# Performance work log

Measured on AMD Instinct MI355X. Metric: run time of the kernel, lower is better.

The kernel has to match this reference:

```python
import jax, jax.numpy as jnp
import numpy as np

M_LEN = 1024
BATCH = 16384


def setup_inputs() -> dict:
    key = jax.random.key(0)
    k0, k1, k2, k3, kw = jax.random.split(key, 5)
    mod0 = jax.random.normal(k0, (BATCH, M_LEN), dtype=jnp.float32)
    mod1 = jax.random.normal(k1, (BATCH, M_LEN), dtype=jnp.float32)
    mod2 = jax.random.normal(k2, (BATCH, M_LEN), dtype=jnp.float32)
    mod3 = jax.random.normal(k3, (BATCH, M_LEN), dtype=jnp.float32)
    # simulate missing modality for first quarter of patients (exercises rescale path)
    mod1 = mod1.at[: BATCH // 4].set(0.0)
    W = jax.random.normal(kw, (M_LEN, M_LEN), dtype=jnp.float32) * (1.0 / np.sqrt(M_LEN))
    return {"mod0": mod0, "mod1": mod1, "mod2": mod2, "mod3": mod3, "W": W}


def reference(mod0, mod1, mod2, mod3, W):
    ndata = jnp.stack([mod0, mod1, mod2, mod3])          # [M, B, L]
    scores = jnp.einsum("mbl,kl->mbk", ndata, W)          # Linear (no bias): x @ W.T
    attention_weights = jax.nn.softmax(scores, axis=0)    # softmax over modalities
    fused = jnp.sum(ndata * attention_weights, axis=0)    # [B, L]
    # vectorized replacement of per-patient python loop:
    # count modalities whose sum is exactly zero; if >0, scale row by (count+1)
    zero_dims = jnp.sum(jnp.sum(ndata, axis=2) == 0.0, axis=0)          # [B] int
    scaler = jnp.where(zero_dims > 0, zero_dims + 1, 1).astype(fused.dtype)
    return fused * scaler[:, None]
```

## Files before the change

kernel.cpp:

```cpp
#include <hip/hip_runtime.h>
#include <hip/hip_bf16.h>

#define M_LEN 1024
#define BATCH 16384

#define BM 128
#define BN 128
#define BK 64
#define THREADS 256

#define BM2 256
#define BN2 256
#define GTHREADS 512

typedef __attribute__((ext_vector_type(8))) short bf16x8;
typedef __attribute__((ext_vector_type(4))) float f32x4;
typedef unsigned short ushort_t;


__device__ __forceinline__ ushort_t bf16_rne(float f) {
    unsigned u = __float_as_uint(f);
    unsigned r = u + 0x7FFFu + ((u >> 16) & 1u);
    return (ushort_t)(r >> 16);
}

__device__ __forceinline__ float bf16_to_f(ushort_t u) {
    return __uint_as_float(((unsigned)u) << 16);
}

__device__ __forceinline__ unsigned pack2(float lo, float hi) {
    return __builtin_amdgcn_perm(__float_as_uint(hi), __float_as_uint(lo), 0x07060302u);
}

__device__ __forceinline__ void gload_lds16(const void* g, void* l) {
    __builtin_amdgcn_global_load_lds(
        (const __attribute__((address_space(1))) unsigned int*)g,
        (__attribute__((address_space(3))) unsigned int*)l,
        16, 0, 0);
}

__device__ __forceinline__ float4 ntload4(const float4* p) {
    f32x4 v = __builtin_nontemporal_load((const f32x4*)p);
    return make_float4(v.x, v.y, v.z, v.w);
}

__global__ __launch_bounds__(THREADS) void convert_pass(
    const float* __restrict__ mod0, const float* __restrict__ mod1,
    const float* __restrict__ mod2, const float* __restrict__ mod3,
    const float* __restrict__ W,
    ushort_t* __restrict__ Ab, ushort_t* __restrict__ Wb, int* __restrict__ zf)
{
    const int blk  = blockIdx.x;
    const int wave = threadIdx.x >> 6;
    const int lane = threadIdx.x & 63;

    if (blk < BATCH) {
        const int b = blk, m = wave;
        const float* mp = (m == 0) ? mod0 : (m == 1) ? mod1 : (m == 2) ? mod2 : mod3;
        const float4* row = (const float4*)(mp + (size_t)b * M_LEN);
        ushort_t* dst = Ab + ((size_t)b * 4 + m) * M_LEN;
        unsigned orr = 0u;
        #pragma unroll
        for (int j = 0; j < 4; ++j) {
            float4 v = ntload4(&row[j * 64 + lane]);
            orr |= (__float_as_uint(v.x) | __float_as_uint(v.y) |
                    __float_as_uint(v.z) | __float_as_uint(v.w)) << 1;
            ushort4 o;
            o.x = bf16_rne(v.x); o.y = bf16_rne(v.y);
            o.z = bf16_rne(v.z); o.w = bf16_rne(v.w);
            ((ushort4*)dst)[j * 64 + lane] = o;
        }
        const int nz = __any(orr != 0u);
        if (lane == 0) zf[b * 4 + m] = nz ? 0 : 1;
    } else {
        const int r = (blk - BATCH) * 4 + wave;
        const float4* row = (const float4*)(W + (size_t)r * M_LEN);
        ushort_t* dst = Wb + (size_t)r * M_LEN;
        #pragma unroll
        for (int j = 0; j < 4; ++j) {
            float4 v = row[j * 64 + lane];
            ushort4 o;
            o.x = bf16_rne(v.x); o.y = bf16_rne(v.y);
            o.z = bf16_rne(v.z); o.w = bf16_rne(v.w);
            ((ushort4*)dst)[j * 64 + lane] = o;
        }
    }
}

__global__ __launch_bounds__(GTHREADS, 2) void gemm_fused3(
    const ushort_t* __restrict__ Ab, const ushort_t* __restrict__ Wb,
    const int* __restrict__ zf, float* __restrict__ out)
{
    __shared__ __align__(16) ushort_t As0[BM2 * BK];
    __shared__ __align__(16) ushort_t Bs0[BN2 * BK];
    __shared__ __align__(16) ushort_t As1[BM2 * BK];
    __shared__ __align__(16) ushort_t Bs1[BN2 * BK];
    __shared__ float scalerS[BM2 / 4];

    const int t    = threadIdx.x;
    const int lane = t & 63;
    const int wave = t >> 6;
    const int quad = lane >> 4;
    const int ln15 = lane & 15;
    const int wm   = wave >> 2;
    const int wn   = wave & 3;

    const int bid  = blockIdx.x;
    const int wid  = (bid & 7) * 128 + (bid >> 3);
    const int colb = wid & 3;
    const int rowb = wid >> 2;
    const int row0 = rowb * BM2;
    const int col0 = colb * BN2;

    if (t < 64) {
        const int4 f = ((const int4*)zf)[rowb * 64 + t];
        const int z = f.x + f.y + f.z + f.w;
        scalerS[t] = (z > 0) ? (float)(z + 1) : 1.0f;
    }

    const int rloc = (lane >> 3);
    const int c8   = (lane & 7) ^ rloc;
    const ushort_t* aP[4];
    const ushort_t* bP[4];
    unsigned dstOff[4];
    #pragma unroll
    for (int q = 0; q < 4; ++q) {
        const int r = wave * 32 + q * 8 + rloc;
        aP[q] = Ab + (size_t)(row0 + r) * M_LEN + c8 * 8;
        bP[q] = Wb + (size_t)(col0 + r) * M_LEN + c8 * 8;
        dstOff[q] = (unsigned)((wave * 32 + q * 8) * 64);
    }

    #define STAGE(AD, BD)                                                   \
        do {                                                                \
            _Pragma("unroll")                                               \
            for (int q = 0; q < 4; ++q) {                                   \
                gload_lds16(aP[q], (AD) + dstOff[q]);                       \
                aP[q] += BK;                                                \
            }                                                               \
            _Pragma("unroll")                                               \
            for (int q = 0; q < 4; ++q) {                                   \
                gload_lds16(bP[q], (BD) + dstOff[q]);                       \
                bP[q] += BK;                                                \
            }                                                               \
        } while (0)

    f32x4 acc[8][4];
    #pragma unroll
    for (int i = 0; i < 8; ++i)
        #pragma unroll
        for (int j = 0; j < 4; ++j)
            acc[i][j] = (f32x4){0.f, 0.f, 0.f, 0.f};

    const unsigned slotB   = (unsigned)(quad ^ (ln15 & 7));
    const unsigned aRowOff = (unsigned)((wm * 128 + ln15) * 64);
    const unsigned bRowOff = (unsigned)((wn * 64 + ln15) * 64);

    auto compute = [&](const ushort_t* As_, const ushort_t* Bs_) {
        #pragma unroll
        for (int ks = 0; ks < 2; ++ks) {
            const unsigned slot8 = (slotB ^ (unsigned)(ks * 4)) * 8u;
            bf16x8 af[8], bfr[4];
            #pragma unroll
            for (int i = 0; i < 8; ++i)
                af[i] = *(const bf16x8*)(&As_[aRowOff + i * 1024 + slot8]);
            #pragma unroll
            for (int j = 0; j < 4; ++j)
                bfr[j] = *(const bf16x8*)(&Bs_[bRowOff + j * 1024 + slot8]);
            #pragma unroll
            for (int i = 0; i < 8; ++i)
                #pragma unroll
                for (int j = 0; j < 4; ++j)
                    acc[i][j] = __builtin_amdgcn_mfma_f32_16x16x32_bf16(
                        af[i], bfr[j], acc[i][j], 0, 0, 0);
        }
    };

    STAGE(As0, Bs0);
    STAGE(As1, Bs1);
    asm volatile("s_waitcnt vmcnt(8) lgkmcnt(0)" ::: "memory");
    __builtin_amdgcn_s_barrier();

    #pragma unroll 1
    for (int t2 = 0; t2 < 7; ++t2) {
        compute(As0, Bs0);
        __builtin_amdgcn_s_barrier();
        STAGE(As0, Bs0);
        asm volatile("s_waitcnt vmcnt(8)" ::: "memory");
        __builtin_amdgcn_s_barrier();

        compute(As1, Bs1);
        __builtin_amdgcn_s_barrier();
        STAGE(As1, Bs1);
        asm volatile("s_waitcnt vmcnt(8)" ::: "memory");
        __builtin_amdgcn_s_barrier();
    }
    compute(As0, Bs0);
    asm volatile("s_waitcnt vmcnt(0)" ::: "memory");
    __builtin_amdgcn_s_barrier();
    compute(As1, Bs1);

    #pragma unroll
    for (int i = 0; i < 8; ++i) {
        const int bl = wm * 32 + i * 4 + quad;
        const int b  = rowb * 64 + bl;
        const float scal = scalerS[bl];
        const ushort_t* xr = Ab + (size_t)b * 4 * M_LEN;
        #pragma unroll
        for (int j = 0; j < 4; ++j) {
            const int k = col0 + wn * 64 + j * 16 + ln15;
            const float x0 = bf16_to_f(xr[k]);
            const float x1 = bf16_to_f(xr[M_LEN + k]);
            const float x2 = bf16_to_f(xr[2 * M_LEN + k]);
            const float x3 = bf16_to_f(xr[3 * M_LEN + k]);
            const f32x4 s = acc[i][j];
            const float mx = fmaxf(fmaxf(s.x, s.y), fmaxf(s.z, s.w));
            const float e0 = __expf(s.x - mx);
            const float e1 = __expf(s.y - mx);
            const float e2 = __expf(s.z - mx);
            const float e3 = __expf(s.w - mx);
            const float num = e0 * x0 + e1 * x1 + e2 * x2 + e3 * x3;
            const float v = num * scal / (e0 + e1 + e2 + e3);
            __builtin_nontemporal_store(v, &out[(size_t)b * M_LEN + k]);
        }
    }
    #undef STAGE
}

__global__ __launch_bounds__(THREADS) void fused_modal_attn(
    const float* __restrict__ mod0, const float* __restrict__ mod1,
    const float* __restrict__ mod2, const float* __restrict__ mod3,
    const float* __restrict__ W, float* __restrict__ out)
{
    __shared__ __align__(16) unsigned short As[BM * BK];
    __shared__ __align__(16) unsigned short Bs[BN * BK];
    __shared__ unsigned rowOr[BM];
    __shared__ float scalerS[BM / 4];

    const int t    = threadIdx.x;
    const int lane = t & 63;
    const int wave = t >> 6;
    const int quad = lane >> 4;
    const int ln15 = lane & 15;
    const int wm   = wave >> 1;
    const int wn   = wave & 1;

    const int colb = blockIdx.x;
    const int rowb = blockIdx.y;
    const int row0 = rowb * BM;
    const int col0 = colb * BN;

    if (t < BM) rowOr[t] = 0u;

    const int sr  = t >> 3;
    const int scl = t & 7;

    const float* ap[4];
    const float* bp[4];
    unsigned ldsOff[4];
    unsigned orAcc[4] = {0u, 0u, 0u, 0u};
    #pragma unroll
    for (int j = 0; j < 4; ++j) {
        const int r  = j * 32 + sr;
        const int gr = row0 + r;
        const int b  = gr >> 2;
        const int m  = gr & 3;
        const float* mp = (m == 0) ? mod0 : (m == 1) ? mod1 : (m == 2) ? mod2 : mod3;
        ap[j] = mp + (size_t)b * M_LEN + scl * 8;
        bp[j] = W + (size_t)(col0 + r) * M_LEN + scl * 8;
        ldsOff[j] = (unsigned)(r * 64 + ((scl ^ (r & 7)) * 8));
    }

    f32x4 acc[4][4];
    #pragma unroll
    for (int i = 0; i < 4; ++i)
        #pragma unroll
        for (int j = 0; j < 4; ++j)
            acc[i][j] = (f32x4){0.f, 0.f, 0.f, 0.f};

    const unsigned slotB   = (unsigned)(quad ^ (ln15 & 7));
    const unsigned aRowOff = (unsigned)((wm * 64 + ln15) * 64);
    const unsigned bRowOff = (unsigned)((wn * 64 + ln15) * 64);

    for (int it = 0; it < 16; ++it) {
        __syncthreads();
        #pragma unroll
        for (int j = 0; j < 4; ++j) {
            const float4* pa = (const float4*)ap[j];
            const float4* pb = (const float4*)bp[j];
            float4 a0 = pa[0], a1 = pa[1];
            float4 b0 = pb[0], b1 = pb[1];
            ap[j] += BK; bp[j] += BK;

            unsigned pA0 = pack2(a0.x, a0.y), pA1 = pack2(a0.z, a0.w);
            unsigned pA2 = pack2(a1.x, a1.y), pA3 = pack2(a1.z, a1.w);
            orAcc[j] |= (pA0 | pA1) | (pA2 | pA3);
            *(uint4*)(&As[ldsOff[j]]) = make_uint4(pA0, pA1, pA2, pA3);

            unsigned pB0 = pack2(b0.x, b0.y), pB1 = pack2(b0.z, b0.w);
            unsigned pB2 = pack2(b1.x, b1.y), pB3 = pack2(b1.z, b1.w);
            *(uint4*)(&Bs[ldsOff[j]]) = make_uint4(pB0, pB1, pB2, pB3);
        }
        __syncthreads();
        #pragma unroll
        for (int ks = 0; ks < 2; ++ks) {
            const unsigned slot8 = (slotB ^ (unsigned)(ks * 4)) * 8u;
            bf16x8 af[4], bfr[4];
            #pragma unroll
            for (int i = 0; i < 4; ++i)
                af[i] = *(const bf16x8*)(&As[aRowOff + i * 1024 + slot8]);
            #pragma unroll
            for (int j = 0; j < 4; ++j)
                bfr[j] = *(const bf16x8*)(&Bs[bRowOff + j * 1024 + slot8]);
            #pragma unroll
            for (int i = 0; i < 4; ++i)
                #pragma unroll
                for (int j = 0; j < 4; ++j)
                    acc[i][j] = __builtin_amdgcn_mfma_f32_16x16x32_bf16(
                        af[i], bfr[j], acc[i][j], 0, 0, 0);
        }
    }

    #pragma unroll
    for (int j = 0; j < 4; ++j)
        atomicOr(&rowOr[j * 32 + sr], orAcc[j]);
    __syncthreads();
    if (t < 32) {
        const int z = (rowOr[4 * t + 0] == 0u) + (rowOr[4 * t + 1] == 0u)
                    + (rowOr[4 * t + 2] == 0u) + (rowOr[4 * t + 3] == 0u);
        scalerS[t] = (z > 0) ? (float)(z + 1) : 1.0f;
    }
    __syncthreads();

    #pragma unroll
    for (int i = 0; i < 4; ++i) {
        const int bl = wm * 16 + i * 4 + quad;
        const int b  = rowb * 32 + bl;
        const float scal = scalerS[bl];
        #pragma unroll
        for (int j = 0; j < 4; ++j) {
            const int k = col0 + wn * 64 + j * 16 + ln15;
            const size_t off = (size_t)b * M_LEN + k;
            const float x0 = mod0[off], x1 = mod1[off];
            const float x2 = mod2[off], x3 = mod3[off];
            const f32x4 s = acc[i][j];
            const float mx = fmaxf(fmaxf(s.x, s.y), fmaxf(s.z, s.w));
            const float e0 = __expf(s.x - mx);
            const float e1 = __expf(s.y - mx);
            const float e2 = __expf(s.z - mx);
            const float e3 = __expf(s.w - mx);
            const float num = e0 * x0 + e1 * x1 + e2 * x2 + e3 * x3;
            out[off] = num * scal / (e0 + e1 + e2 + e3);
        }
    }
}

extern "C" void kernel_launch(void* const* d_in, const int* in_sizes, int n_in,
                              void* d_out, int out_size, void* d_ws, size_t ws_size,
                              hipStream_t stream) {
    const float* mod0 = (const float*)d_in[0];
    const float* mod1 = (const float*)d_in[1];
    const float* mod2 = (const float*)d_in[2];
    const float* mod3 = (const float*)d_in[3];
    const float* W    = (const float*)d_in[4];
    float* out = (float*)d_out;

    const size_t abBytes = (size_t)4 * BATCH * M_LEN * sizeof(ushort_t);
    const size_t wbBytes = (size_t)M_LEN * M_LEN * sizeof(ushort_t);
    const size_t zfBytes = (size_t)4 * BATCH * sizeof(int);
    const size_t need = abBytes + wbBytes + zfBytes;

    if (ws_size >= need) {
        ushort_t* Ab = (ushort_t*)d_ws;
        ushort_t* Wb = (ushort_t*)((char*)d_ws + abBytes);
        int*      zfp = (int*)((char*)d_ws + abBytes + wbBytes);

        convert_pass<<<dim3(BATCH + M_LEN / 4), dim3(THREADS), 0, stream>>>(
            mod0, mod1, mod2, mod3, W, Ab, Wb, zfp);

        gemm_fused3<<<dim3((M_LEN / BN2) * ((4 * BATCH) / BM2)), dim3(GTHREADS), 0, stream>>>(
            Ab, Wb, zfp, out);
    } else {
        dim3 grid(M_LEN / BN, (4 * BATCH) / BM);
        fused_modal_attn<<<grid, dim3(THREADS), 0, stream>>>(
            mod0, mod1, mod2, mod3, W, out);
    }
}
```

Before: 384.2 us.

## Fuse fp32-to-bf16 activation conversion and zero-row detection into the GEMM kernel

```diff
diff --git a/kernel.cpp b/kernel.cpp
--- a/kernel.cpp
+++ b/kernel.cpp
@@ -22,10 +22,6 @@
     unsigned u = __float_as_uint(f);
     unsigned r = u + 0x7FFFu + ((u >> 16) & 1u);
     return (ushort_t)(r >> 16);
-}
-
-__device__ __forceinline__ float bf16_to_f(ushort_t u) {
-    return __uint_as_float(((unsigned)u) << 16);
 }
 
 __device__ __forceinline__ unsigned pack2(float lo, float hi) {
@@ -39,62 +35,34 @@
         16, 0, 0);
 }
 
-__device__ __forceinline__ float4 ntload4(const float4* p) {
-    f32x4 v = __builtin_nontemporal_load((const f32x4*)p);
-    return make_float4(v.x, v.y, v.z, v.w);
-}
-
-__global__ __launch_bounds__(THREADS) void convert_pass(
+__global__ __launch_bounds__(THREADS) void convert_w(
+    const float* __restrict__ W, ushort_t* __restrict__ Wb)
+{
+    const int wave = threadIdx.x >> 6;
+    const int lane = threadIdx.x & 63;
+    const int r = blockIdx.x * 4 + wave;
+    const float4* row = (const float4*)(W + (size_t)r * M_LEN);
+    ushort_t* dst = Wb + (size_t)r * M_LEN;
+    #pragma unroll
+    for (int j = 0; j < 4; ++j) {
+        float4 v = row[j * 64 + lane];
+        ushort4 o;
+        o.x = bf16_rne(v.x); o.y = bf16_rne(v.y);
+        o.z = bf16_rne(v.z); o.w = bf16_rne(v.w);
+        ((ushort4*)dst)[j * 64 + lane] = o;
+    }
+}
+
+__global__ __launch_bounds__(GTHREADS, 2) void fused_big(
     const float* __restrict__ mod0, const float* __restrict__ mod1,
     const float* __restrict__ mod2, const float* __restrict__ mod3,
-    const float* __restrict__ W,
-    ushort_t* __restrict__ Ab, ushort_t* __restrict__ Wb, int* __restrict__ zf)
-{
-    const int blk  = blockIdx.x;
-    const int wave = threadIdx.x >> 6;
-    const int lane = threadIdx.x & 63;
-
-    if (blk < BATCH) {
-        const int b = blk, m = wave;
-        const float* mp = (m == 0) ? mod0 : (m == 1) ? mod1 : (m == 2) ? mod2 : mod3;
-        const float4* row = (const float4*)(mp + (size_t)b * M_LEN);
-        ushort_t* dst = Ab + ((size_t)b * 4 + m) * M_LEN;
-        unsigned orr = 0u;
-        #pragma unroll
-        for (int j = 0; j < 4; ++j) {
-            float4 v = ntload4(&row[j * 64 + lane]);
-            orr |= (__float_as_uint(v.x) | __float_as_uint(v.y) |
-                    __float_as_uint(v.z) | __float_as_uint(v.w)) << 1;
-            ushort4 o;
-            o.x = bf16_rne(v.x); o.y = bf16_rne(v.y);
-            o.z = bf16_rne(v.z); o.w = bf16_rne(v.w);
-            ((ushort4*)dst)[j * 64 + lane] = o;
-        }
-        const int nz = __any(orr != 0u);
-        if (lane == 0) zf[b * 4 + m] = nz ? 0 : 1;
-    } else {
-        const int r = (blk - BATCH) * 4 + wave;
-        const float4* row = (const float4*)(W + (size_t)r * M_LEN);
-        ushort_t* dst = Wb + (size_t)r * M_LEN;
-        #pragma unroll
-        for (int j = 0; j < 4; ++j) {
-            float4 v = row[j * 64 + lane];
-            ushort4 o;
-            o.x = bf16_rne(v.x); o.y = bf16_rne(v.y);
-            o.z = bf16_rne(v.z); o.w = bf16_rne(v.w);
-            ((ushort4*)dst)[j * 64 + lane] = o;
-        }
-    }
-}
-
-__global__ __launch_bounds__(GTHREADS, 2) void gemm_fused3(
-    const ushort_t* __restrict__ Ab, const ushort_t* __restrict__ Wb,
-    const int* __restrict__ zf, float* __restrict__ out)
+    const ushort_t* __restrict__ Wb, float* __restrict__ out)
 {
     __shared__ __align__(16) ushort_t As0[BM2 * BK];
     __shared__ __align__(16) ushort_t Bs0[BN2 * BK];
     __shared__ __align__(16) ushort_t As1[BM2 * BK];
     __shared__ __align__(16) ushort_t Bs1[BN2 * BK];
+    __shared__ unsigned rowOr[BM2];
     __shared__ float scalerS[BM2 / 4];
 
     const int t    = threadIdx.x;
@@ -112,38 +80,62 @@
     const int row0 = rowb * BM2;
     const int col0 = colb * BN2;
 
-    if (t < 64) {
-        const int4 f = ((const int4*)zf)[rowb * 64 + t];
-        const int z = f.x + f.y + f.z + f.w;
-        scalerS[t] = (z > 0) ? (float)(z + 1) : 1.0f;
-    }
+    if (t < BM2) rowOr[t] = 0u;
 
     const int rloc = (lane >> 3);
     const int c8   = (lane & 7) ^ rloc;
-    const ushort_t* aP[4];
+    const float*    aFp[4];
     const ushort_t* bP[4];
-    unsigned dstOff[4];
+    unsigned wrOff[4];
+    unsigned dstB[4];
+    unsigned orAcc[4] = {0u, 0u, 0u, 0u};
     #pragma unroll
     for (int q = 0; q < 4; ++q) {
-        const int r = wave * 32 + q * 8 + rloc;
-        aP[q] = Ab + (size_t)(row0 + r) * M_LEN + c8 * 8;
-        bP[q] = Wb + (size_t)(col0 + r) * M_LEN + c8 * 8;
-        dstOff[q] = (unsigned)((wave * 32 + q * 8) * 64);
-    }
-
-    #define STAGE(AD, BD)                                                   \
-        do {                                                                \
-            _Pragma("unroll")                                               \
-            for (int q = 0; q < 4; ++q) {                                   \
-                gload_lds16(aP[q], (AD) + dstOff[q]);                       \
-                aP[q] += BK;                                                \
-            }                                                               \
-            _Pragma("unroll")                                               \
-            for (int q = 0; q < 4; ++q) {                                   \
-                gload_lds16(bP[q], (BD) + dstOff[q]);                       \
-                bP[q] += BK;                                                \
-            }                                                               \
-        } while (0)
+        const int r  = wave * 32 + q * 8 + rloc;
+        const int gr = row0 + r;
+        const int bb = gr >> 2;
+        const int mm = gr & 3;
+        const float* mp = (mm == 0) ? mod0 : (mm == 1) ? mod1 : (mm == 2) ? mod2 : mod3;
+        aFp[q] = mp + (size_t)bb * M_LEN + c8 * 8;
+        bP[q]  = Wb + (size_t)(col0 + r) * M_LEN + c8 * 8;
+        wrOff[q] = (unsigned)(r * 64 + (lane & 7) * 8);
+        dstB[q]  = (unsigned)((wave * 32 + q * 8) * 64);
+    }
+
+    float4 aR[8];
+
+    auto aIssue = [&]() {
+        #pragma unroll
+        for (int q = 0; q < 4; ++q) {
+            const float4* pa = (const float4*)aFp[q];
+            aR[2 * q]     = pa[0];
+            aR[2 * q + 1] = pa[1];
+            aFp[q] += BK;
+        }
+    };
+    auto aCvt = [&](ushort_t* dA) {
+        #pragma unroll
+        for (int q = 0; q < 4; ++q) {
+            const float4 v0 = aR[2 * q], v1 = aR[2 * q + 1];
+            orAcc[q] |= ((__float_as_uint(v0.x) | __float_as_uint(v0.y) |
+                          __float_as_uint(v0.z) | __float_as_uint(v0.w) |
+                          __float_as_uint(v1.x) | __float_as_uint(v1.y) |
+                          __float_as_uint(v1.z) | __float_as_uint(v1.w)) << 1);
+            unsigned p0, p1, p2, p3;
+            asm("v_cvt_pk_bf16_f32 %0, %1, %2" : "=v"(p0) : "v"(v0.x), "v"(v0.y));
+            asm("v_cvt_pk_bf16_f32 %0, %1, %2" : "=v"(p1) : "v"(v0.z), "v"(v0.w));
+            asm("v_cvt_pk_bf16_f32 %0, %1, %2" : "=v"(p2) : "v"(v1.x), "v"(v1.y));
+            asm("v_cvt_pk_bf16_f32 %0, %1, %2" : "=v"(p3) : "v"(v1.z), "v"(v1.w));
+            *(uint4*)&dA[wrOff[q]] = make_uint4(p0, p1, p2, p3);
+        }
+    };
+    auto bIssue = [&](ushort_t* dB) {
+        #pragma unroll
+        for (int q = 0; q < 4; ++q) {
+            gload_lds16(bP[q], dB + dstB[q]);
+            bP[q] += BK;
+        }
+    };
 
     f32x4 acc[8][4];
     #pragma unroll
@@ -176,43 +168,73 @@
         }
     };
 
-    STAGE(As0, Bs0);
-    STAGE(As1, Bs1);
-    asm volatile("s_waitcnt vmcnt(8) lgkmcnt(0)" ::: "memory");
+    aIssue();
+    bIssue(Bs0);
+    aCvt(As0);
+    aIssue();
+    bIssue(Bs1);
+    asm volatile("s_waitcnt vmcnt(12)" ::: "memory");
+    asm volatile("s_waitcnt lgkmcnt(0)" ::: "memory");
     __builtin_amdgcn_s_barrier();
+    asm volatile("" ::: "memory");
 
     #pragma unroll 1
-    for (int t2 = 0; t2 < 7; ++t2) {
+    for (int it = 0; it < 7; ++it) {
         compute(As0, Bs0);
         __builtin_amdgcn_s_barrier();
-        STAGE(As0, Bs0);
-        asm volatile("s_waitcnt vmcnt(8)" ::: "memory");
+        asm volatile("" ::: "memory");
+        aCvt(As1);
+        aIssue();
+        bIssue(Bs0);
+        asm volatile("s_waitcnt vmcnt(12)" ::: "memory");
+        asm volatile("s_waitcnt lgkmcnt(0)" ::: "memory");
         __builtin_amdgcn_s_barrier();
+        asm volatile("" ::: "memory");
 
         compute(As1, Bs1);
         __builtin_amdgcn_s_barrier();
-        STAGE(As1, Bs1);
-        asm volatile("s_waitcnt vmcnt(8)" ::: "memory");
+        asm volatile("" ::: "memory");
+        aCvt(As0);
+        aIssue();
+        bIssue(Bs1);
+        asm volatile("s_waitcnt vmcnt(12)" ::: "memory");
+        asm volatile("s_waitcnt lgkmcnt(0)" ::: "memory");
         __builtin_amdgcn_s_barrier();
-    }
+        asm volatile("" ::: "memory");
+    }
+
     compute(As0, Bs0);
+    __builtin_amdgcn_s_barrier();
+    asm volatile("" ::: "memory");
+    aCvt(As1);
     asm volatile("s_waitcnt vmcnt(0)" ::: "memory");
+    asm volatile("s_waitcnt lgkmcnt(0)" ::: "memory");
     __builtin_amdgcn_s_barrier();
+    asm volatile("" ::: "memory");
     compute(As1, Bs1);
+
+    #pragma unroll
+    for (int q = 0; q < 4; ++q)
+        atomicOr(&rowOr[wave * 32 + q * 8 + rloc], orAcc[q]);
+    __syncthreads();
+    if (t < 64) {
+        const int z = (rowOr[4 * t + 0] == 0u) + (rowOr[4 * t + 1] == 0u)
+                    + (rowOr[4 * t + 2] == 0u) + (rowOr[4 * t + 3] == 0u);
+        scalerS[t] = (z > 0) ? (float)(z + 1) : 1.0f;
+    }
+    __syncthreads();
 
     #pragma unroll
     for (int i = 0; i < 8; ++i) {
         const int bl = wm * 32 + i * 4 + quad;
         const int b  = rowb * 64 + bl;
         const float scal = scalerS[bl];
-        const ushort_t* xr = Ab + (size_t)b * 4 * M_LEN;
         #pragma unroll
         for (int j = 0; j < 4; ++j) {
             const int k = col0 + wn * 64 + j * 16 + ln15;
-            const float x0 = bf16_to_f(xr[k]);
-            const float x1 = bf16_to_f(xr[M_LEN + k]);
-            const float x2 = bf16_to_f(xr[2 * M_LEN + k]);
-            const float x3 = bf16_to_f(xr[3 * M_LEN + k]);
+            const size_t off = (size_t)b * M_LEN + k;
+            const float x0 = mod0[off], x1 = mod1[off];
+            const float x2 = mod2[off], x3 = mod3[off];
             const f32x4 s = acc[i][j];
             const float mx = fmaxf(fmaxf(s.x, s.y), fmaxf(s.z, s.w));
             const float e0 = __expf(s.x - mx);
@@ -221,10 +243,9 @@
             const float e3 = __expf(s.w - mx);
             const float num = e0 * x0 + e1 * x1 + e2 * x2 + e3 * x3;
             const float v = num * scal / (e0 + e1 + e2 + e3);
-            __builtin_nontemporal_store(v, &out[(size_t)b * M_LEN + k]);
-        }
-    }
-    #undef STAGE
+            __builtin_nontemporal_store(v, &out[off]);
+        }
+    }
 }
 
 __global__ __launch_bounds__(THREADS) void fused_modal_attn(
@@ -365,21 +386,13 @@
     const float* W    = (const float*)d_in[4];
     float* out = (float*)d_out;
 
-    const size_t abBytes = (size_t)4 * BATCH * M_LEN * sizeof(ushort_t);
     const size_t wbBytes = (size_t)M_LEN * M_LEN * sizeof(ushort_t);
-    const size_t zfBytes = (size_t)4 * BATCH * sizeof(int);
-    const size_t need = abBytes + wbBytes + zfBytes;
-
-    if (ws_size >= need) {
-        ushort_t* Ab = (ushort_t*)d_ws;
-        ushort_t* Wb = (ushort_t*)((char*)d_ws + abBytes);
-        int*      zfp = (int*)((char*)d_ws + abBytes + wbBytes);
-
-        convert_pass<<<dim3(BATCH + M_LEN / 4), dim3(THREADS), 0, stream>>>(
-            mod0, mod1, mod2, mod3, W, Ab, Wb, zfp);
-
-        gemm_fused3<<<dim3((M_LEN / BN2) * ((4 * BATCH) / BM2)), dim3(GTHREADS), 0, stream>>>(
-            Ab, Wb, zfp, out);
+
+    if (ws_size >= wbBytes) {
+        ushort_t* Wb = (ushort_t*)d_ws;
+        convert_w<<<dim3(M_LEN / 4), dim3(THREADS), 0, stream>>>(W, Wb);
+        fused_big<<<dim3((M_LEN / BN2) * ((4 * BATCH) / BM2)), dim3(GTHREADS), 0, stream>>>(
+            mod0, mod1, mod2, mod3, Wb, out);
     } else {
         dim3 grid(M_LEN / BN, (4 * BATCH) / BM);
         fused_modal_attn<<<grid, dim3(THREADS), 0, stream>>>(
```

Result: slower. 606.1 us (+57.8%).

## Restructure GEMM main loop into triple-buffered BK=32 pipeline with interleaved loads

Applied to the files above, without the earlier changes.

```diff
diff --git a/kernel.cpp b/kernel.cpp
--- a/kernel.cpp
+++ b/kernel.cpp
@@ -11,6 +11,7 @@
 
 #define BM2 256
 #define BN2 256
+#define BK2 32
 #define GTHREADS 512
 
 typedef __attribute__((ext_vector_type(8))) short bf16x8;
@@ -87,14 +88,12 @@
     }
 }
 
-__global__ __launch_bounds__(GTHREADS, 2) void gemm_fused3(
+__global__ __launch_bounds__(GTHREADS, 2) void gemm_8p(
     const ushort_t* __restrict__ Ab, const ushort_t* __restrict__ Wb,
     const int* __restrict__ zf, float* __restrict__ out)
 {
-    __shared__ __align__(16) ushort_t As0[BM2 * BK];
-    __shared__ __align__(16) ushort_t Bs0[BN2 * BK];
-    __shared__ __align__(16) ushort_t As1[BM2 * BK];
-    __shared__ __align__(16) ushort_t Bs1[BN2 * BK];
+    __shared__ __align__(16) ushort_t AsB[3][BM2 * BK2];
+    __shared__ __align__(16) ushort_t BsB[3][BN2 * BK2];
     __shared__ float scalerS[BM2 / 4];
 
     const int t    = threadIdx.x;
@@ -118,32 +117,18 @@
         scalerS[t] = (z > 0) ? (float)(z + 1) : 1.0f;
     }
 
-    const int rloc = (lane >> 3);
-    const int c8   = (lane & 7) ^ rloc;
-    const ushort_t* aP[4];
-    const ushort_t* bP[4];
-    unsigned dstOff[4];
-    #pragma unroll
-    for (int q = 0; q < 4; ++q) {
-        const int r = wave * 32 + q * 8 + rloc;
-        aP[q] = Ab + (size_t)(row0 + r) * M_LEN + c8 * 8;
-        bP[q] = Wb + (size_t)(col0 + r) * M_LEN + c8 * 8;
-        dstOff[q] = (unsigned)((wave * 32 + q * 8) * 64);
-    }
-
-    #define STAGE(AD, BD)                                                   \
-        do {                                                                \
-            _Pragma("unroll")                                               \
-            for (int q = 0; q < 4; ++q) {                                   \
-                gload_lds16(aP[q], (AD) + dstOff[q]);                       \
-                aP[q] += BK;                                                \
-            }                                                               \
-            _Pragma("unroll")                                               \
-            for (int q = 0; q < 4; ++q) {                                   \
-                gload_lds16(bP[q], (BD) + dstOff[q]);                       \
-                bP[q] += BK;                                                \
-            }                                                               \
-        } while (0)
+    const int rloc = lane >> 2;
+    const int c4   = (lane & 3) ^ (rloc & 3);
+    const ushort_t* aP[2];
+    const ushort_t* bP[2];
+    unsigned dstOff[2];
+    #pragma unroll
+    for (int g = 0; g < 2; ++g) {
+        const int r = wave * 32 + g * 16 + rloc;
+        aP[g] = Ab + (size_t)(row0 + r) * M_LEN + c4 * 8;
+        bP[g] = Wb + (size_t)(col0 + r) * M_LEN + c4 * 8;
+        dstOff[g] = (unsigned)((wave * 32 + g * 16) * BK2);
+    }
 
     f32x4 acc[8][4];
     #pragma unroll
@@ -152,53 +137,82 @@
         for (int j = 0; j < 4; ++j)
             acc[i][j] = (f32x4){0.f, 0.f, 0.f, 0.f};
 
-    const unsigned slotB   = (unsigned)(quad ^ (ln15 & 7));
-    const unsigned aRowOff = (unsigned)((wm * 128 + ln15) * 64);
-    const unsigned bRowOff = (unsigned)((wn * 64 + ln15) * 64);
-
-    auto compute = [&](const ushort_t* As_, const ushort_t* Bs_) {
-        #pragma unroll
-        for (int ks = 0; ks < 2; ++ks) {
-            const unsigned slot8 = (slotB ^ (unsigned)(ks * 4)) * 8u;
-            bf16x8 af[8], bfr[4];
-            #pragma unroll
-            for (int i = 0; i < 8; ++i)
-                af[i] = *(const bf16x8*)(&As_[aRowOff + i * 1024 + slot8]);
+    const unsigned slotOff = (unsigned)((quad ^ (ln15 & 3)) * 8);
+    const unsigned aRowOff = (unsigned)((wm * 128 + ln15) * BK2);
+    const unsigned bRowOff = (unsigned)((wn * 64 + ln15) * BK2);
+
+    auto tile_body = [&](const ushort_t* cA, const ushort_t* cB,
+                         ushort_t* sA, ushort_t* sB, bool stage) {
+        bf16x8 af[4], bfr[4];
+        #pragma unroll
+        for (int j = 0; j < 4; ++j)
+            bfr[j] = *(const bf16x8*)&cB[bRowOff + j * 16 * BK2 + slotOff];
+        #pragma unroll
+        for (int i = 0; i < 4; ++i)
+            af[i] = *(const bf16x8*)&cA[aRowOff + i * 16 * BK2 + slotOff];
+        if (stage) {
+            #pragma unroll
+            for (int g = 0; g < 2; ++g) {
+                gload_lds16(aP[g], sA + dstOff[g]);
+                aP[g] += BK2;
+            }
+        }
+        __builtin_amdgcn_s_setprio(1);
+        #pragma unroll
+        for (int i = 0; i < 4; ++i)
             #pragma unroll
             for (int j = 0; j < 4; ++j)
-                bfr[j] = *(const bf16x8*)(&Bs_[bRowOff + j * 1024 + slot8]);
-            #pragma unroll
-            for (int i = 0; i < 8; ++i)
-                #pragma unroll
-                for (int j = 0; j < 4; ++j)
-                    acc[i][j] = __builtin_amdgcn_mfma_f32_16x16x32_bf16(
-                        af[i], bfr[j], acc[i][j], 0, 0, 0);
-        }
+                acc[i][j] = __builtin_amdgcn_mfma_f32_16x16x32_bf16(
+                    af[i], bfr[j], acc[i][j], 0, 0, 0);
+        __builtin_amdgcn_s_setprio(0);
+        __builtin_amdgcn_s_barrier();
+        #pragma unroll
+        for (int i = 0; i < 4; ++i)
+            af[i] = *(const bf16x8*)&cA[aRowOff + (4 + i) * 16 * BK2 + slotOff];
+        if (stage) {
+            #pragma unroll
+            for (int g = 0; g < 2; ++g) {
+                gload_lds16(bP[g], sB + dstOff[g]);
+                bP[g] += BK2;
+            }
+        }
+        __builtin_amdgcn_s_setprio(1);
+        #pragma unroll
+        for (int i = 0; i < 4; ++i)
+            #pragma unroll
+            for (int j = 0; j < 4; ++j)
+                acc[4 + i][j] = __builtin_amdgcn_mfma_f32_16x16x32_bf16(
+                    af[i], bfr[j], acc[4 + i][j], 0, 0, 0);
+        __builtin_amdgcn_s_setprio(0);
     };
 
-    STAGE(As0, Bs0);
-    STAGE(As1, Bs1);
-    asm volatile("s_waitcnt vmcnt(8) lgkmcnt(0)" ::: "memory");
+    ushort_t *A0 = AsB[0], *A1 = AsB[1], *A2 = AsB[2];
+    ushort_t *B0 = BsB[0], *B1 = BsB[1], *B2 = BsB[2];
+
+    #pragma unroll
+    for (int g = 0; g < 2; ++g) { gload_lds16(aP[g], A0 + dstOff[g]); aP[g] += BK2; }
+    #pragma unroll
+    for (int g = 0; g < 2; ++g) { gload_lds16(bP[g], B0 + dstOff[g]); bP[g] += BK2; }
+    #pragma unroll
+    for (int g = 0; g < 2; ++g) { gload_lds16(aP[g], A1 + dstOff[g]); aP[g] += BK2; }
+    #pragma unroll
+    for (int g = 0; g < 2; ++g) { gload_lds16(bP[g], B1 + dstOff[g]); bP[g] += BK2; }
+    asm volatile("s_waitcnt vmcnt(4) lgkmcnt(0)" ::: "memory");
     __builtin_amdgcn_s_barrier();
 
     #pragma unroll 1
-    for (int t2 = 0; t2 < 7; ++t2) {
-        compute(As0, Bs0);
+    for (int kt = 0; kt < 30; ++kt) {
+        tile_body(A0, B0, A2, B2, true);
+        asm volatile("s_waitcnt vmcnt(4)" ::: "memory");
         __builtin_amdgcn_s_barrier();
-        STAGE(As0, Bs0);
-        asm volatile("s_waitcnt vmcnt(8)" ::: "memory");
-        __builtin_amdgcn_s_barrier();
-
-        compute(As1, Bs1);
-        __builtin_amdgcn_s_barrier();
-        STAGE(As1, Bs1);
-        asm volatile("s_waitcnt vmcnt(8)" ::: "memory");
-        __builtin_amdgcn_s_barrier();
-    }
-    compute(As0, Bs0);
+        ushort_t* x;
+        x = A0; A0 = A1; A1 = A2; A2 = x;
+        x = B0; B0 = B1; B1 = B2; B2 = x;
+    }
+    tile_body(A0, B0, (ushort_t*)0, (ushort_t*)0, false);
     asm volatile("s_waitcnt vmcnt(0)" ::: "memory");
     __builtin_amdgcn_s_barrier();
-    compute(As1, Bs1);
+    tile_body(A1, B1, (ushort_t*)0, (ushort_t*)0, false);
 
     #pragma unroll
     for (int i = 0; i < 8; ++i) {
@@ -224,7 +238,6 @@
             __builtin_nontemporal_store(v, &out[(size_t)b * M_LEN + k]);
         }
     }
-    #undef STAGE
 }
 
 __global__ __launch_bounds__(THREADS) void fused_modal_attn(
@@ -378,7 +391,7 @@
         convert_pass<<<dim3(BATCH + M_LEN / 4), dim3(THREADS), 0, stream>>>(
             mod0, mod1, mod2, mod3, W, Ab, Wb, zfp);
 
-        gemm_fused3<<<dim3((M_LEN / BN2) * ((4 * BATCH) / BM2)), dim3(GTHREADS), 0, stream>>>(
+        gemm_8p<<<dim3((M_LEN / BN2) * ((4 * BATCH) / BM2)), dim3(GTHREADS), 0, stream>>>(
             Ab, Wb, zfp, out);
     } else {
         dim3 grid(M_LEN / BN, (4 * BATCH) / BM);
```

Measured after the change: 374.3 us. -2.6%, faster.
